# Performance work log

Measured on AMD Instinct MI355X. Metric: run time of the kernel, lower is better.

Reference implementation:

```python
import jax, jax.numpy as jnp
import numpy as np


def _logsparse_mask(L, win_len):
    # Allowed: causal (dist >= 0) AND (within local window OR dist is a power of 2)
    i = jnp.arange(L, dtype=jnp.int32)[:, None]
    j = jnp.arange(L, dtype=jnp.int32)[None, :]
    dist = i - j
    pow2 = (dist > 0) & ((dist & (dist - 1)) == 0)
    return (dist >= 0) & ((dist <= win_len) | pow2)  # [L, L] bool


def setup_inputs() -> dict:
    key = jax.random.key(0)
    kq, kk, kv = jax.random.split(key, 3)
    B, H, L, E = 4, 8, 4096, 64
    return {
        "q": jax.random.normal(kq, (B, H, L, E), dtype=jnp.float32),
        "k": jax.random.normal(kk, (B, H, L, E), dtype=jnp.float32),
        "v": jax.random.normal(kv, (B, H, L, E), dtype=jnp.float32),
        "win_len": 32,
    }


def reference(q, k, v, win_len):
    B, H, L, E = q.shape
    scale = 1.0 / jnp.sqrt(jnp.asarray(E, dtype=q.dtype))
    # [B, H, Lq, Lk] raw attention scores
    scores = jnp.einsum("bhqe,bhke->bhqk", q, k) * scale
    mask = _logsparse_mask(L, win_len)  # [L, L] bool, broadcast over B, H
    neg = jnp.asarray(-jnp.inf, dtype=scores.dtype)
    scores = jnp.where(mask[None, None], scores, neg)
    attn = jax.nn.softmax(scores, axis=-1)  # every row has >=1 allowed key (dist 0)
    out = jnp.einsum("bhqk,bhke->bhqe", attn, v)
    return out
```

## Files before the change

### kernel.cpp

```cpp
#include <hip/hip_runtime.h>


constexpr int L     = 4096;
constexpr int E     = 64;
constexpr int QPB   = 64;
constexpr int WMAX  = 32;
constexpr int WROWS = QPB + WMAX;
constexpr int RS    = 160;
constexpr int CS    = 40;
constexpr int VOFF  = WROWS * RS;
constexpr int TPB   = L / QPB;
constexpr int NP2   = 6;

typedef _Float16 h2  __attribute__((ext_vector_type(2)));
typedef __fp16   h2c __attribute__((ext_vector_type(2)));

__device__ __forceinline__ h2 pkrtz(float a, float b) {
    h2c r = __builtin_amdgcn_cvt_pkrtz(a, b);
    return __builtin_bit_cast(h2, r);
}

#if defined(__has_builtin)
#if __has_builtin(__builtin_amdgcn_fdot2)
#define HAVE_FDOT2 1
#endif
#endif

__device__ __forceinline__ float fdot2h(h2 a, h2 b, float c) {
#ifdef HAVE_FDOT2
    return __builtin_amdgcn_fdot2(__builtin_bit_cast(h2c, a),
                                  __builtin_bit_cast(h2c, b), c, false);
#else
    return fmaf((float)a.x, (float)b.x, fmaf((float)a.y, (float)b.y, c));
#endif
}

__device__ __forceinline__ h2 as_h2(unsigned u) {
    return __builtin_bit_cast(h2, u);
}
__device__ __forceinline__ unsigned as_u32(h2 h) {
    return __builtin_bit_cast(unsigned, h);
}

template<int CTRL>
__device__ __forceinline__ float dppf(float x) {
    return __int_as_float(__builtin_amdgcn_update_dpp(
        0, __float_as_int(x), CTRL, 0xF, 0xF, true));
}
__device__ __forceinline__ float quad_sum(float x) {
    x += dppf<0xB1>(x);
    x += dppf<0x4E>(x);
    return x;
}
__device__ __forceinline__ float quad_max(float x) {
    x = fmaxf(x, dppf<0xB1>(x));
    x = fmaxf(x, dppf<0x4E>(x));
    return x;
}
__device__ __forceinline__ float quad_bcast(float x, int r) {
    switch (r & 3) {
    case 0:  return dppf<0x00>(x);
    case 1:  return dppf<0x55>(x);
    case 2:  return dppf<0xAA>(x);
    default: return dppf<0xFF>(x);
    }
}

__global__ __launch_bounds__(256) void logsparse_attn(
    const float* __restrict__ q,
    const float* __restrict__ k,
    const float* __restrict__ v,
    float* __restrict__ out,
    const int* __restrict__ win_ptr)
{
    __shared__ alignas(16) unsigned char buf[2 * WROWS * RS];

    const int bid = blockIdx.x, nb = gridDim.x;
    int swz = bid;
    if ((nb & 7) == 0) {
        const int cpx = nb >> 3;
        swz = (bid & 7) * cpx + (bid >> 3);
    }
    const int bh  = swz / TPB;
    const int t   = (swz % TPB) * QPB;
    const int tid = threadIdx.x;
    const int qid = tid >> 2;
    const int s   = tid & 3;
    const int i   = t + qid;
    const int ce  = s * 16;
    int win = *win_ptr; win = min(win, WMAX);

    const size_t base = (size_t)bh * (L * E);
    const float* kb = k + base;
    const float* vb = v + base;

    h2 qh[8];
    {
        const float* qp = q + base + (size_t)i * E + ce;
        #pragma unroll
        for (int u = 0; u < 4; ++u) {
            float4 f = *(const float4*)(qp + u * 4);
            qh[u*2+0] = pkrtz(f.x * 0.125f, f.y * 0.125f);
            qh[u*2+1] = pkrtz(f.z * 0.125f, f.w * 0.125f);
        }
    }

    #pragma unroll
    for (int it = 0; it < 6; ++it) {
        int idx = tid + it * 256;
        int r = idx >> 4, w = idx & 15;
        int cc = w >> 2, p = w & 3;
        int j = max(t - WMAX + r, 0);
        float4 fk = *(const float4*)(kb + (size_t)j * E + w * 4);
        float4 fv = *(const float4*)(vb + (size_t)j * E + w * 4);
        uint2 pk; pk.x = as_u32(pkrtz(fk.x, fk.y)); pk.y = as_u32(pkrtz(fk.z, fk.w));
        uint2 pv; pv.x = as_u32(pkrtz(fv.x, fv.y)); pv.y = as_u32(pkrtz(fv.z, fv.w));
        *(uint2*)(buf + r * RS + cc * CS + p * 8) = pk;
        *(uint2*)(buf + VOFF + r * RS + cc * CS + p * 8) = pv;
    }
    __syncthreads();

    float ws[9];
    float wp[2];
    #pragma unroll
    for (int kk = 0; kk < 9; ++kk) ws[kk] = -60000.f;
    wp[0] = wp[1] = -60000.f;

    #pragma unroll
    for (int o = 0; o <= WMAX; ++o) {
        const unsigned char* rp = buf + (qid + WMAX - o) * RS + s * CS;
        uint2 u0 = *(const uint2*)(rp);
        uint2 u1 = *(const uint2*)(rp + 8);
        uint2 u2 = *(const uint2*)(rp + 16);
        uint2 u3 = *(const uint2*)(rp + 24);
        float a0 = 0.f, a1 = 0.f;
        a0 = fdot2h(as_h2(u0.x), qh[0], a0); a1 = fdot2h(as_h2(u0.y), qh[1], a1);
        a0 = fdot2h(as_h2(u1.x), qh[2], a0); a1 = fdot2h(as_h2(u1.y), qh[3], a1);
        a0 = fdot2h(as_h2(u2.x), qh[4], a0); a1 = fdot2h(as_h2(u2.y), qh[5], a1);
        a0 = fdot2h(as_h2(u3.x), qh[6], a0); a1 = fdot2h(as_h2(u3.y), qh[7], a1);
        float sv = quad_sum(a0 + a1);
        const bool isp2  = (o > 0) && ((o & (o - 1)) == 0);
        const bool valid = ((o <= win) || isp2) && (o <= i);
        sv = valid ? sv : -60000.f;
        if (s == (o & 3)) ws[o >> 2] = sv;
    }

    #pragma unroll
    for (int dd = 0; dd < NP2; ++dd) {
        const int d = 64 << dd;
        if (t + QPB - 1 >= d) {
            const int j = max(i - d, 0);
            const float* kr = kb + (size_t)j * E + ce;
            float a0 = 0.f, a1 = 0.f;
            #pragma unroll
            for (int u = 0; u < 4; ++u) {
                float4 f = *(const float4*)(kr + u * 4);
                a0 = fdot2h(pkrtz(f.x, f.y), qh[u*2+0], a0);
                a1 = fdot2h(pkrtz(f.z, f.w), qh[u*2+1], a1);
            }
            float sv = quad_sum(a0 + a1);
            sv = (i >= d) ? sv : -60000.f;
            if (s == ((WMAX + 1 + dd) & 3)) wp[dd < 4 ? 0 : 1] = sv;
        }
    }

    float ml = ws[0];
    #pragma unroll
    for (int kk = 1; kk < 9; ++kk) ml = fmaxf(ml, ws[kk]);
    ml = fmaxf(ml, fmaxf(wp[0], wp[1]));
    const float m = quad_max(ml);

    float ew[9], ep0, ep1, dl = 0.f;
    #pragma unroll
    for (int kk = 0; kk < 9; ++kk) { ew[kk] = __expf(ws[kk] - m); dl += ew[kk]; }
    ep0 = __expf(wp[0] - m); ep1 = __expf(wp[1] - m); dl += ep0 + ep1;
    const float inv = 1.0f / quad_sum(dl);
    #pragma unroll
    for (int kk = 0; kk < 9; ++kk) ew[kk] *= inv;
    ep0 *= inv; ep1 *= inv;

    h2 ah[8];
    #pragma unroll
    for (int j = 0; j < 8; ++j) ah[j] = h2{(_Float16)0.f, (_Float16)0.f};

    #pragma unroll
    for (int o = 0; o <= WMAX; ++o) {
        const float pd = quad_bcast(ew[o >> 2], o & 3);
        const h2 pdh = pkrtz(pd, pd);
        const unsigned char* rp = buf + VOFF + (qid + WMAX - o) * RS + s * CS;
        uint2 u0 = *(const uint2*)(rp);
        uint2 u1 = *(const uint2*)(rp + 8);
        uint2 u2 = *(const uint2*)(rp + 16);
        uint2 u3 = *(const uint2*)(rp + 24);
        ah[0] += as_h2(u0.x) * pdh; ah[1] += as_h2(u0.y) * pdh;
        ah[2] += as_h2(u1.x) * pdh; ah[3] += as_h2(u1.y) * pdh;
        ah[4] += as_h2(u2.x) * pdh; ah[5] += as_h2(u2.y) * pdh;
        ah[6] += as_h2(u3.x) * pdh; ah[7] += as_h2(u3.y) * pdh;
    }

    #pragma unroll
    for (int dd = 0; dd < NP2; ++dd) {
        const int d = 64 << dd;
        if (t + QPB - 1 >= d) {
            const float pd = quad_bcast(dd < 4 ? ep0 : ep1, (WMAX + 1 + dd) & 3);
            const h2 pdh = pkrtz(pd, pd);
            const int j = max(i - d, 0);
            const float* vr = vb + (size_t)j * E + ce;
            #pragma unroll
            for (int u = 0; u < 4; ++u) {
                float4 f = *(const float4*)(vr + u * 4);
                ah[u*2+0] += pkrtz(f.x, f.y) * pdh;
                ah[u*2+1] += pkrtz(f.z, f.w) * pdh;
            }
        }
    }

    float* op = out + base + (size_t)i * E + ce;
    #pragma unroll
    for (int u = 0; u < 4; ++u) {
        float4 o4;
        o4.x = (float)ah[u*2+0].x; o4.y = (float)ah[u*2+0].y;
        o4.z = (float)ah[u*2+1].x; o4.w = (float)ah[u*2+1].y;
        *(float4*)(op + u * 4) = o4;
    }
}

extern "C" void kernel_launch(void* const* d_in, const int* in_sizes, int n_in,
                              void* d_out, int out_size, void* d_ws, size_t ws_size,
                              hipStream_t stream) {
    const float* q = (const float*)d_in[0];
    const float* k = (const float*)d_in[1];
    const float* v = (const float*)d_in[2];
    const int* win = (const int*)d_in[3];
    float* out = (float*)d_out;

    const int n_rows = in_sizes[0] / E;
    const int blocks = n_rows / QPB;
    logsparse_attn<<<blocks, 256, 0, stream>>>(q, k, v, out, win);
}
```

Baseline: 48.64 us.

## Overlap global power-of-two loads with LDS staging and software-pipeline window loops

Moves the power-of-two-offset K score computation (global loads) ahead of the barrier so its latency overlaps the shared-memory staging. It also adds 4-deep register prefetching of LDS rows in both the QK and PV window loops, and double-buffers the global V loads for the power-of-two offsets, issuing them before the window PV loop. This is meant to hide global and LDS latency in exchange for higher register pressure, which could lower occupancy.

```diff
diff --git a/kernel.cpp b/kernel.cpp
--- a/kernel.cpp
+++ b/kernel.cpp
@@ -118,33 +118,9 @@
         *(uint2*)(buf + r * RS + cc * CS + p * 8) = pk;
         *(uint2*)(buf + VOFF + r * RS + cc * CS + p * 8) = pv;
     }
-    __syncthreads();
-
-    float ws[9];
+
     float wp[2];
-    #pragma unroll
-    for (int kk = 0; kk < 9; ++kk) ws[kk] = -60000.f;
     wp[0] = wp[1] = -60000.f;
-
-    #pragma unroll
-    for (int o = 0; o <= WMAX; ++o) {
-        const unsigned char* rp = buf + (qid + WMAX - o) * RS + s * CS;
-        uint2 u0 = *(const uint2*)(rp);
-        uint2 u1 = *(const uint2*)(rp + 8);
-        uint2 u2 = *(const uint2*)(rp + 16);
-        uint2 u3 = *(const uint2*)(rp + 24);
-        float a0 = 0.f, a1 = 0.f;
-        a0 = fdot2h(as_h2(u0.x), qh[0], a0); a1 = fdot2h(as_h2(u0.y), qh[1], a1);
-        a0 = fdot2h(as_h2(u1.x), qh[2], a0); a1 = fdot2h(as_h2(u1.y), qh[3], a1);
-        a0 = fdot2h(as_h2(u2.x), qh[4], a0); a1 = fdot2h(as_h2(u2.y), qh[5], a1);
-        a0 = fdot2h(as_h2(u3.x), qh[6], a0); a1 = fdot2h(as_h2(u3.y), qh[7], a1);
-        float sv = quad_sum(a0 + a1);
-        const bool isp2  = (o > 0) && ((o & (o - 1)) == 0);
-        const bool valid = ((o <= win) || isp2) && (o <= i);
-        sv = valid ? sv : -60000.f;
-        if (s == (o & 3)) ws[o >> 2] = sv;
-    }
-
     #pragma unroll
     for (int dd = 0; dd < NP2; ++dd) {
         const int d = 64 << dd;
@@ -164,6 +140,46 @@
         }
     }
 
+    __syncthreads();
+
+    float ws[9];
+    #pragma unroll
+    for (int kk = 0; kk < 9; ++kk) ws[kk] = -60000.f;
+
+    uint2 pf[4][4];
+    #pragma unroll
+    for (int o = 0; o < 4; ++o) {
+        const unsigned char* rp = buf + (qid + WMAX - o) * RS + s * CS;
+        pf[o][0] = *(const uint2*)(rp);
+        pf[o][1] = *(const uint2*)(rp + 8);
+        pf[o][2] = *(const uint2*)(rp + 16);
+        pf[o][3] = *(const uint2*)(rp + 24);
+    }
+    #pragma unroll
+    for (int o = 0; o <= WMAX; ++o) {
+        float a0 = 0.f, a1 = 0.f;
+        a0 = fdot2h(as_h2(pf[o & 3][0].x), qh[0], a0);
+        a1 = fdot2h(as_h2(pf[o & 3][0].y), qh[1], a1);
+        a0 = fdot2h(as_h2(pf[o & 3][1].x), qh[2], a0);
+        a1 = fdot2h(as_h2(pf[o & 3][1].y), qh[3], a1);
+        a0 = fdot2h(as_h2(pf[o & 3][2].x), qh[4], a0);
+        a1 = fdot2h(as_h2(pf[o & 3][2].y), qh[5], a1);
+        a0 = fdot2h(as_h2(pf[o & 3][3].x), qh[6], a0);
+        a1 = fdot2h(as_h2(pf[o & 3][3].y), qh[7], a1);
+        float sv = quad_sum(a0 + a1);
+        const bool isp2  = (o > 0) && ((o & (o - 1)) == 0);
+        const bool valid = ((o <= win) || isp2) && (o <= i);
+        sv = valid ? sv : -60000.f;
+        if (s == (o & 3)) ws[o >> 2] = sv;
+        if (o + 4 <= WMAX) {
+            const unsigned char* rp = buf + (qid + WMAX - (o + 4)) * RS + s * CS;
+            pf[o & 3][0] = *(const uint2*)(rp);
+            pf[o & 3][1] = *(const uint2*)(rp + 8);
+            pf[o & 3][2] = *(const uint2*)(rp + 16);
+            pf[o & 3][3] = *(const uint2*)(rp + 24);
+        }
+    }
+
     float ml = ws[0];
     #pragma unroll
     for (int kk = 1; kk < 9; ++kk) ml = fmaxf(ml, ws[kk]);
@@ -179,23 +195,45 @@
     for (int kk = 0; kk < 9; ++kk) ew[kk] *= inv;
     ep0 *= inv; ep1 *= inv;
 
+    float4 vpf[2][4];
+    #pragma unroll
+    for (int dd = 0; dd < 2; ++dd) {
+        if (t + QPB - 1 >= (64 << dd)) {
+            const float* vr = vb + (size_t)max(i - (64 << dd), 0) * E + ce;
+            vpf[dd][0] = *(const float4*)(vr);
+            vpf[dd][1] = *(const float4*)(vr + 4);
+            vpf[dd][2] = *(const float4*)(vr + 8);
+            vpf[dd][3] = *(const float4*)(vr + 12);
+        }
+    }
+
     h2 ah[8];
     #pragma unroll
     for (int j = 0; j < 8; ++j) ah[j] = h2{(_Float16)0.f, (_Float16)0.f};
 
+    #pragma unroll
+    for (int o = 0; o < 4; ++o) {
+        const unsigned char* rp = buf + VOFF + (qid + WMAX - o) * RS + s * CS;
+        pf[o][0] = *(const uint2*)(rp);
+        pf[o][1] = *(const uint2*)(rp + 8);
+        pf[o][2] = *(const uint2*)(rp + 16);
+        pf[o][3] = *(const uint2*)(rp + 24);
+    }
     #pragma unroll
     for (int o = 0; o <= WMAX; ++o) {
         const float pd = quad_bcast(ew[o >> 2], o & 3);
         const h2 pdh = pkrtz(pd, pd);
-        const unsigned char* rp = buf + VOFF + (qid + WMAX - o) * RS + s * CS;
-        uint2 u0 = *(const uint2*)(rp);
-        uint2 u1 = *(const uint2*)(rp + 8);
-        uint2 u2 = *(const uint2*)(rp + 16);
-        uint2 u3 = *(const uint2*)(rp + 24);
-        ah[0] += as_h2(u0.x) * pdh; ah[1] += as_h2(u0.y) * pdh;
-        ah[2] += as_h2(u1.x) * pdh; ah[3] += as_h2(u1.y) * pdh;
-        ah[4] += as_h2(u2.x) * pdh; ah[5] += as_h2(u2.y) * pdh;
-        ah[6] += as_h2(u3.x) * pdh; ah[7] += as_h2(u3.y) * pdh;
+        ah[0] += as_h2(pf[o & 3][0].x) * pdh; ah[1] += as_h2(pf[o & 3][0].y) * pdh;
+        ah[2] += as_h2(pf[o & 3][1].x) * pdh; ah[3] += as_h2(pf[o & 3][1].y) * pdh;
+        ah[4] += as_h2(pf[o & 3][2].x) * pdh; ah[5] += as_h2(pf[o & 3][2].y) * pdh;
+        ah[6] += as_h2(pf[o & 3][3].x) * pdh; ah[7] += as_h2(pf[o & 3][3].y) * pdh;
+        if (o + 4 <= WMAX) {
+            const unsigned char* rp = buf + VOFF + (qid + WMAX - (o + 4)) * RS + s * CS;
+            pf[o & 3][0] = *(const uint2*)(rp);
+            pf[o & 3][1] = *(const uint2*)(rp + 8);
+            pf[o & 3][2] = *(const uint2*)(rp + 16);
+            pf[o & 3][3] = *(const uint2*)(rp + 24);
+        }
     }
 
     #pragma unroll
@@ -204,14 +242,19 @@
         if (t + QPB - 1 >= d) {
             const float pd = quad_bcast(dd < 4 ? ep0 : ep1, (WMAX + 1 + dd) & 3);
             const h2 pdh = pkrtz(pd, pd);
-            const int j = max(i - d, 0);
-            const float* vr = vb + (size_t)j * E + ce;
             #pragma unroll
             for (int u = 0; u < 4; ++u) {
-                float4 f = *(const float4*)(vr + u * 4);
+                float4 f = vpf[dd & 1][u];
                 ah[u*2+0] += pkrtz(f.x, f.y) * pdh;
                 ah[u*2+1] += pkrtz(f.z, f.w) * pdh;
             }
+        }
+        if (dd + 2 < NP2 && t + QPB - 1 >= (64 << (dd + 2))) {
+            const float* vr = vb + (size_t)max(i - (64 << (dd + 2)), 0) * E + ce;
+            vpf[dd & 1][0] = *(const float4*)(vr);
+            vpf[dd & 1][1] = *(const float4*)(vr + 4);
+            vpf[dd & 1][2] = *(const float4*)(vr + 8);
+            vpf[dd & 1][3] = *(const float4*)(vr + 12);
         }
     }
 
```

Measured after the change: 43.40 us (median of 2 runs). 1.12x faster.

## Use wavefront-uniform LDS band rows and move syncthreads after global pow2 loads

Applied to the files above, without the earlier changes.

The local-window loops now walk a fixed band of 48 rows that starts at each 16-query group's base row instead of a per-thread shifted row. All lanes in a group therefore read the same LDS rows, which turns reads into broadcasts and makes addresses uniform, but each thread computes 48 dot products instead of 33 and masks out the extras. The barrier is also moved after the global-memory power-of-two score loads so those loads overlap the LDS staging. Register use grows because of the 12-element score array.

```diff
diff --git a/kernel.cpp b/kernel.cpp
--- a/kernel.cpp
+++ b/kernel.cpp
@@ -11,6 +11,7 @@
 constexpr int VOFF  = WROWS * RS;
 constexpr int TPB   = L / QPB;
 constexpr int NP2   = 6;
+constexpr int BAND  = 48;
 
 typedef _Float16 h2  __attribute__((ext_vector_type(2)));
 typedef __fp16   h2c __attribute__((ext_vector_type(2)));
@@ -86,6 +87,8 @@
     const int tid = threadIdx.x;
     const int qid = tid >> 2;
     const int s   = tid & 3;
+    const int ql  = qid & 15;
+    const int wb  = qid & ~15;
     const int i   = t + qid;
     const int ce  = s * 16;
     int win = *win_ptr; win = min(win, WMAX);
@@ -118,33 +121,9 @@
         *(uint2*)(buf + r * RS + cc * CS + p * 8) = pk;
         *(uint2*)(buf + VOFF + r * RS + cc * CS + p * 8) = pv;
     }
-    __syncthreads();
-
-    float ws[9];
+
     float wp[2];
-    #pragma unroll
-    for (int kk = 0; kk < 9; ++kk) ws[kk] = -60000.f;
     wp[0] = wp[1] = -60000.f;
-
-    #pragma unroll
-    for (int o = 0; o <= WMAX; ++o) {
-        const unsigned char* rp = buf + (qid + WMAX - o) * RS + s * CS;
-        uint2 u0 = *(const uint2*)(rp);
-        uint2 u1 = *(const uint2*)(rp + 8);
-        uint2 u2 = *(const uint2*)(rp + 16);
-        uint2 u3 = *(const uint2*)(rp + 24);
-        float a0 = 0.f, a1 = 0.f;
-        a0 = fdot2h(as_h2(u0.x), qh[0], a0); a1 = fdot2h(as_h2(u0.y), qh[1], a1);
-        a0 = fdot2h(as_h2(u1.x), qh[2], a0); a1 = fdot2h(as_h2(u1.y), qh[3], a1);
-        a0 = fdot2h(as_h2(u2.x), qh[4], a0); a1 = fdot2h(as_h2(u2.y), qh[5], a1);
-        a0 = fdot2h(as_h2(u3.x), qh[6], a0); a1 = fdot2h(as_h2(u3.y), qh[7], a1);
-        float sv = quad_sum(a0 + a1);
-        const bool isp2  = (o > 0) && ((o & (o - 1)) == 0);
-        const bool valid = ((o <= win) || isp2) && (o <= i);
-        sv = valid ? sv : -60000.f;
-        if (s == (o & 3)) ws[o >> 2] = sv;
-    }
-
     #pragma unroll
     for (int dd = 0; dd < NP2; ++dd) {
         const int d = 64 << dd;
@@ -164,19 +143,46 @@
         }
     }
 
-    float ml = ws[0];
-    #pragma unroll
-    for (int kk = 1; kk < 9; ++kk) ml = fmaxf(ml, ws[kk]);
+    __syncthreads();
+
+    float ss[12];
+    #pragma unroll
+    for (int kk = 0; kk < 12; ++kk) ss[kk] = -60000.f;
+
+    #pragma unroll
+    for (int r_off = 0; r_off < BAND; ++r_off) {
+        const unsigned char* rp = buf + (wb + r_off) * RS + s * CS;
+        uint2 u0 = *(const uint2*)(rp);
+        uint2 u1 = *(const uint2*)(rp + 8);
+        uint2 u2 = *(const uint2*)(rp + 16);
+        uint2 u3 = *(const uint2*)(rp + 24);
+        float a0 = 0.f, a1 = 0.f;
+        a0 = fdot2h(as_h2(u0.x), qh[0], a0); a1 = fdot2h(as_h2(u0.y), qh[1], a1);
+        a0 = fdot2h(as_h2(u1.x), qh[2], a0); a1 = fdot2h(as_h2(u1.y), qh[3], a1);
+        a0 = fdot2h(as_h2(u2.x), qh[4], a0); a1 = fdot2h(as_h2(u2.y), qh[5], a1);
+        a0 = fdot2h(as_h2(u3.x), qh[6], a0); a1 = fdot2h(as_h2(u3.y), qh[7], a1);
+        float sv = quad_sum(a0 + a1);
+        const int o = ql + 32 - r_off;
+        const bool isp2  = (o > 0) && ((o & (o - 1)) == 0);
+        const bool valid = (o >= 0) && (o <= WMAX) && (o <= i)
+                           && ((o <= win) || isp2);
+        sv = valid ? sv : -60000.f;
+        if (s == (r_off & 3)) ss[r_off >> 2] = sv;
+    }
+
+    float ml = ss[0];
+    #pragma unroll
+    for (int kk = 1; kk < 12; ++kk) ml = fmaxf(ml, ss[kk]);
     ml = fmaxf(ml, fmaxf(wp[0], wp[1]));
     const float m = quad_max(ml);
 
-    float ew[9], ep0, ep1, dl = 0.f;
-    #pragma unroll
-    for (int kk = 0; kk < 9; ++kk) { ew[kk] = __expf(ws[kk] - m); dl += ew[kk]; }
+    float ep0, ep1, dl = 0.f;
+    #pragma unroll
+    for (int kk = 0; kk < 12; ++kk) { ss[kk] = __expf(ss[kk] - m); dl += ss[kk]; }
     ep0 = __expf(wp[0] - m); ep1 = __expf(wp[1] - m); dl += ep0 + ep1;
     const float inv = 1.0f / quad_sum(dl);
     #pragma unroll
-    for (int kk = 0; kk < 9; ++kk) ew[kk] *= inv;
+    for (int kk = 0; kk < 12; ++kk) ss[kk] *= inv;
     ep0 *= inv; ep1 *= inv;
 
     h2 ah[8];
@@ -184,10 +190,10 @@
     for (int j = 0; j < 8; ++j) ah[j] = h2{(_Float16)0.f, (_Float16)0.f};
 
     #pragma unroll
-    for (int o = 0; o <= WMAX; ++o) {
-        const float pd = quad_bcast(ew[o >> 2], o & 3);
+    for (int r_off = 0; r_off < BAND; ++r_off) {
+        const float pd = quad_bcast(ss[r_off >> 2], r_off & 3);
         const h2 pdh = pkrtz(pd, pd);
-        const unsigned char* rp = buf + VOFF + (qid + WMAX - o) * RS + s * CS;
+        const unsigned char* rp = buf + VOFF + (wb + r_off) * RS + s * CS;
         uint2 u0 = *(const uint2*)(rp);
         uint2 u1 = *(const uint2*)(rp + 8);
         uint2 u2 = *(const uint2*)(rp + 16);
```

Measured after the change: 49.97 us. 2.7% more time.
